# Kernel tuning notes

Hardware: AMD Instinct MI355X
Metric: run time of the kernel (lower is better)

The kernel has to match this reference:

```python
import jax, jax.numpy as jnp
import numpy as np

NEG_SLOPE = 0.2
EPS = 1e-16

N_NODES = 50000
N_EDGES = 800000
N_QUERY = 100000


def setup_inputs() -> dict:
    key = jax.random.key(0)
    ks = jax.random.split(key, 12)
    x = jax.random.normal(ks[0], (N_NODES, 128), dtype=jnp.float32)
    edge_index = jax.random.randint(ks[1], (2, N_EDGES), 0, N_NODES, dtype=jnp.int64)
    edge_label_index = jax.random.randint(ks[2], (2, N_QUERY), 0, N_NODES, dtype=jnp.int64)
    # layer 1: in=128 -> out=256, heads=4, per-head dim 64
    W1 = jax.random.normal(ks[3], (128, 256), dtype=jnp.float32) * 0.08
    a1_src = jax.random.normal(ks[4], (4, 64), dtype=jnp.float32) * 0.08
    a1_dst = jax.random.normal(ks[5], (4, 64), dtype=jnp.float32) * 0.08
    b1 = jnp.zeros((256,), dtype=jnp.float32)
    # layer 2: in=256 -> out=32, heads=2, per-head dim 16
    W2 = jax.random.normal(ks[6], (256, 32), dtype=jnp.float32) * 0.08
    a2_src = jax.random.normal(ks[7], (2, 16), dtype=jnp.float32) * 0.08
    a2_dst = jax.random.normal(ks[8], (2, 16), dtype=jnp.float32) * 0.08
    b2 = jnp.zeros((32,), dtype=jnp.float32)
    return {"x": x, "edge_index": edge_index, "edge_label_index": edge_label_index,
            "W1": W1, "a1_src": a1_src, "a1_dst": a1_dst, "b1": b1,
            "W2": W2, "a2_src": a2_src, "a2_dst": a2_dst, "b2": b2}


def gat_layer(x, src, dst, W, a_src, a_dst, b, heads):
    """Multi-head GAT: gather -> edge logits -> segment softmax over dst -> scatter-add."""
    n = x.shape[0]
    out = W.shape[1]
    c = out // heads
    h = (x @ W).reshape(n, heads, c)                       # [N,H,C]
    # per-node attention contributions: [N,H]
    alpha_s = jnp.einsum('nhc,hc->nh', h, a_src)
    alpha_d = jnp.einsum('nhc,hc->nh', h, a_dst)
    e = alpha_s[src] + alpha_d[dst]                         # [E,H]
    e = jax.nn.leaky_relu(e, NEG_SLOPE)
    # segment softmax over incoming edges of each dst node
    m = jax.ops.segment_max(e, dst, num_segments=n)         # [N,H]
    m = jnp.where(jnp.isfinite(m), m, 0.0)
    ex = jnp.exp(e - m[dst])                                # [E,H]
    s = jax.ops.segment_sum(ex, dst, num_segments=n)        # [N,H]
    w = ex / (s[dst] + EPS)                                 # [E,H]
    msg = h[src] * w[:, :, None]                            # [E,H,C]
    agg = jax.ops.segment_sum(msg, dst, num_segments=n)     # [N,H,C]
    return agg.reshape(n, out) + b


def reference(x, edge_index, edge_label_index, W1, a1_src, a1_dst, b1, W2, a2_src, a2_dst, b2):
    n = x.shape[0]
    loops = jnp.arange(n, dtype=edge_index.dtype)
    src = jnp.concatenate([edge_index[0], loops])
    dst = jnp.concatenate([edge_index[1], loops])
    # encode (dropout p=0 and use_bn=False are identities)
    z = gat_layer(x, src, dst, W1, a1_src, a1_dst, b1, heads=4)
    z = jax.nn.relu(z)
    z = gat_layer(z, src, dst, W2, a2_src, a2_dst, b2, heads=2)
    # decode: dot product of endpoint embeddings
    return (z[edge_label_index[0]] * z[edge_label_index[1]]).sum(axis=-1)
```

## Files before the change

### kernel.cpp

```cpp
#include <hip/hip_runtime.h>

#define NEG_SLOPE 0.2f
#define EPSV 1e-16f

__device__ __forceinline__ float lrelu(float e){ return (e > 0.f) ? e : NEG_SLOPE*e; }
__device__ __forceinline__ float bf2f(unsigned short u){ return __uint_as_float((unsigned)u << 16); }
__device__ __forceinline__ unsigned short f2bf(float f){
  unsigned u = __float_as_uint(f);
  u += 0x7FFFu + ((u >> 16) & 1u);
  return (unsigned short)(u >> 16);
}

__global__ void k_deg(const int* __restrict__ ei, int E, int N, int* __restrict__ deg){
  int t = blockIdx.x*blockDim.x + threadIdx.x;
  int ET = E + N;
  if (t >= ET) return;
  int dst = (t < E) ? ei[E + t] : (t - E);
  atomicAdd(&deg[dst], 1);
}

__global__ void k_scan(const int* __restrict__ deg, int N, int* __restrict__ rs){
  __shared__ int sums[1024];
  int tid = threadIdx.x;
  int chunk = (N + 1023) >> 10;
  int s = tid*chunk, e = min(s+chunk, N);
  int sum = 0;
  for (int i = s; i < e; ++i) sum += deg[i];
  sums[tid] = sum;
  __syncthreads();
  for (int off = 1; off < 1024; off <<= 1){
    int v = (tid >= off) ? sums[tid-off] : 0;
    __syncthreads();
    sums[tid] += v;
    __syncthreads();
  }
  int run = (tid == 0) ? 0 : sums[tid-1];
  for (int i = s; i < e; ++i){ rs[i] = run; run += deg[i]; }
  if (tid == 1023) rs[N] = run;
}

__global__ void k_fill(const int* __restrict__ ei, int E, int N,
                       const int* __restrict__ rs, int* __restrict__ cnt,
                       int* __restrict__ csr_s){
  int t = blockIdx.x*blockDim.x + threadIdx.x;
  int ET = E + N;
  if (t >= ET) return;
  int src, dst;
  if (t < E){ src = ei[t]; dst = ei[E + t]; } else { src = dst = t - E; }
  int pos = atomicAdd(&cnt[dst], 1);
  csr_s[rs[dst] + pos] = src;
}

__global__ __launch_bounds__(256) void k_gemm1(const float* __restrict__ x, const float* __restrict__ W1,
                                               const float* __restrict__ a1s, const float* __restrict__ a1d,
                                               int N, unsigned short* __restrict__ h1b,
                                               float* __restrict__ als, float* __restrict__ ald){
  __shared__ float xs[8][128];
  int bn = blockIdx.x * 8;
  int tid = threadIdx.x;
  {
    int m = tid >> 5, k4 = tid & 31;
    int node = bn + m;
    float4 v = (node < N) ? ((const float4*)x)[(size_t)node*32 + k4]
                          : make_float4(0.f,0.f,0.f,0.f);
    ((float4*)xs[m])[k4] = v;
  }
  __syncthreads();
  float acc[8];
  #pragma unroll
  for (int m = 0; m < 8; ++m) acc[m] = 0.f;
  int j = tid;
  for (int k = 0; k < 128; ++k){
    float w = W1[k*256 + j];
    #pragma unroll
    for (int m = 0; m < 8; ++m) acc[m] = fmaf(xs[m][k], w, acc[m]);
  }
  int head = j >> 6;
  int lane = j & 63;
  float cas = a1s[head*64 + lane];
  float cad = a1d[head*64 + lane];
  #pragma unroll
  for (int m = 0; m < 8; ++m){
    int node = bn + m;
    if (node < N) h1b[(size_t)node*256 + j] = f2bf(acc[m]);
    float vs = acc[m]*cas, vd = acc[m]*cad;
    #pragma unroll
    for (int o = 32; o; o >>= 1){ vs += __shfl_xor(vs, o, 64); vd += __shfl_xor(vd, o, 64); }
    if (lane == 0 && node < N){ als[node*4+head] = vs; ald[node*4+head] = vd; }
  }
}

__global__ __launch_bounds__(256) void k_gemm2(const float* __restrict__ z1, const float* __restrict__ W2,
                                               const float* __restrict__ a2s, const float* __restrict__ a2d,
                                               int N, float* __restrict__ h2,
                                               float* __restrict__ als, float* __restrict__ ald){
  __shared__ float zs[8][256];
  int bn = blockIdx.x * 8;
  int tid = threadIdx.x;
  {
    int m = tid >> 6, k4 = tid & 63;
    int node = bn + m;
    const float4 zero = make_float4(0.f,0.f,0.f,0.f);
    ((float4*)zs[m])[k4]      = (node < N)   ? ((const float4*)z1)[(size_t)node*64 + k4] : zero;
    int m2 = m + 4, node2 = bn + m2;
    ((float4*)zs[m2])[k4]     = (node2 < N)  ? ((const float4*)z1)[(size_t)node2*64 + k4] : zero;
  }
  __syncthreads();
  int j = tid & 31;
  int m = tid >> 5;
  float acc = 0.f;
  for (int k = 0; k < 256; ++k) acc = fmaf(zs[m][k], W2[k*32 + j], acc);
  int node = bn + m;
  int head = j >> 4, lane = j & 15;
  if (node < N) h2[(size_t)node*32 + j] = acc;
  float vs = acc * a2s[head*16 + lane];
  float vd = acc * a2d[head*16 + lane];
  #pragma unroll
  for (int o = 8; o; o >>= 1){ vs += __shfl_xor(vs, o, 64); vd += __shfl_xor(vd, o, 64); }
  if (lane == 0 && node < N){ als[node*2+head] = vs; ald[node*2+head] = vd; }
}

__global__ __launch_bounds__(256) void k_agg1(const int* __restrict__ rs, const int* __restrict__ csr_s,
                                              const float* __restrict__ als, const float* __restrict__ ald,
                                              const unsigned short* __restrict__ h1b, const float* __restrict__ b1,
                                              int N, float* __restrict__ z1){
  __shared__ int    sidx[256];
  __shared__ float  sexp[256*4];
  __shared__ float4 accl[4][64];
  __shared__ float  sl[4][64];
  int node = blockIdx.x;
  int tid = threadIdx.x;
  int w = tid >> 6, lane = tid & 63;
  int head = lane >> 4;
  int beg = rs[node], end = rs[node+1];
  const ushort4* h1v = (const ushort4*)h1b;
  float4 acc = make_float4(0.f,0.f,0.f,0.f);
  float s = 0.f;
  for (int base = beg; base < end; base += 256){
    int cnt = min(256, end - base);
    if (tid < cnt) sidx[tid] = csr_s[base + tid];
    __syncthreads();
    for (int t = tid; t < cnt*4; t += 256){
      int e = t >> 2, h = t & 3;
      int sv = sidx[e];
      sexp[t] = __expf(lrelu(als[sv*4 + h] + ald[node*4 + h]));
    }
    __syncthreads();
    int e = w;
    for (; e + 12 < cnt; e += 16){
      int s0 = sidx[e], s1 = sidx[e+4], s2 = sidx[e+8], s3 = sidx[e+12];
      float x0 = sexp[e*4+head], x1 = sexp[(e+4)*4+head];
      float x2 = sexp[(e+8)*4+head], x3 = sexp[(e+12)*4+head];
      ushort4 u0 = h1v[(size_t)s0*64 + lane];
      ushort4 u1 = h1v[(size_t)s1*64 + lane];
      ushort4 u2 = h1v[(size_t)s2*64 + lane];
      ushort4 u3 = h1v[(size_t)s3*64 + lane];
      acc.x = fmaf(bf2f(u0.x), x0, acc.x); acc.y = fmaf(bf2f(u0.y), x0, acc.y);
      acc.z = fmaf(bf2f(u0.z), x0, acc.z); acc.w = fmaf(bf2f(u0.w), x0, acc.w);
      acc.x = fmaf(bf2f(u1.x), x1, acc.x); acc.y = fmaf(bf2f(u1.y), x1, acc.y);
      acc.z = fmaf(bf2f(u1.z), x1, acc.z); acc.w = fmaf(bf2f(u1.w), x1, acc.w);
      acc.x = fmaf(bf2f(u2.x), x2, acc.x); acc.y = fmaf(bf2f(u2.y), x2, acc.y);
      acc.z = fmaf(bf2f(u2.z), x2, acc.z); acc.w = fmaf(bf2f(u2.w), x2, acc.w);
      acc.x = fmaf(bf2f(u3.x), x3, acc.x); acc.y = fmaf(bf2f(u3.y), x3, acc.y);
      acc.z = fmaf(bf2f(u3.z), x3, acc.z); acc.w = fmaf(bf2f(u3.w), x3, acc.w);
      s += (x0 + x1) + (x2 + x3);
    }
    for (; e < cnt; e += 4){
      int s0 = sidx[e];
      float x0 = sexp[e*4+head];
      ushort4 u0 = h1v[(size_t)s0*64 + lane];
      acc.x = fmaf(bf2f(u0.x), x0, acc.x); acc.y = fmaf(bf2f(u0.y), x0, acc.y);
      acc.z = fmaf(bf2f(u0.z), x0, acc.z); acc.w = fmaf(bf2f(u0.w), x0, acc.w);
      s += x0;
    }
    __syncthreads();
  }
  accl[w][lane] = acc;
  sl[w][lane] = s;
  __syncthreads();
  if (tid < 64){
    float4 a0 = accl[0][tid], a1 = accl[1][tid], a2 = accl[2][tid], a3 = accl[3][tid];
    float st = sl[0][tid] + sl[1][tid] + sl[2][tid] + sl[3][tid];
    float inv = 1.0f / (st + EPSV);
    float4 bb = ((const float4*)b1)[tid];
    float4 r;
    r.x = fmaf(a0.x + a1.x + a2.x + a3.x, inv, bb.x);
    r.y = fmaf(a0.y + a1.y + a2.y + a3.y, inv, bb.y);
    r.z = fmaf(a0.z + a1.z + a2.z + a3.z, inv, bb.z);
    r.w = fmaf(a0.w + a1.w + a2.w + a3.w, inv, bb.w);
    r.x = fmaxf(r.x, 0.f); r.y = fmaxf(r.y, 0.f);
    r.z = fmaxf(r.z, 0.f); r.w = fmaxf(r.w, 0.f);
    ((float4*)z1)[(size_t)node*64 + tid] = r;
  }
}

__global__ __launch_bounds__(256) void k_agg2(const int* __restrict__ rs, const int* __restrict__ csr_s,
                                              const float* __restrict__ als, const float* __restrict__ ald,
                                              const float* __restrict__ h2, const float* __restrict__ b2,
                                              int N, float* __restrict__ z2){
  int tid = threadIdx.x;
  int node = blockIdx.x*4 + (tid >> 6);
  if (node >= N) return;
  int lane = tid & 63;
  int slot = lane >> 3;
  int q    = lane & 7;
  int head = q >> 2;
  float aldn = ald[node*2 + head];
  int beg = rs[node], end = rs[node+1];
  float4 acc = make_float4(0.f,0.f,0.f,0.f);
  float s = 0.f;
  for (int i = beg + slot; i < end; i += 8){
    int s0 = csr_s[i];
    float x0 = __expf(lrelu(als[s0*2+head] + aldn));
    float4 v0 = ((const float4*)h2)[(size_t)s0*8 + q];
    acc.x = fmaf(v0.x, x0, acc.x); acc.y = fmaf(v0.y, x0, acc.y);
    acc.z = fmaf(v0.z, x0, acc.z); acc.w = fmaf(v0.w, x0, acc.w);
    s += x0;
  }
  #pragma unroll
  for (int o = 8; o < 64; o <<= 1){
    acc.x += __shfl_xor(acc.x, o, 64); acc.y += __shfl_xor(acc.y, o, 64);
    acc.z += __shfl_xor(acc.z, o, 64); acc.w += __shfl_xor(acc.w, o, 64);
    s += __shfl_xor(s, o, 64);
  }
  if (slot == 0){
    float inv = 1.0f / (s + EPSV);
    float4 bb = ((const float4*)b2)[q];
    float4 r;
    r.x = fmaf(acc.x, inv, bb.x); r.y = fmaf(acc.y, inv, bb.y);
    r.z = fmaf(acc.z, inv, bb.z); r.w = fmaf(acc.w, inv, bb.w);
    ((float4*)z2)[(size_t)node*8 + q] = r;
  }
}

__global__ void k_decode(const int* __restrict__ eli, int NQ,
                         const float* __restrict__ z2, float* __restrict__ out){
  int t = blockIdx.x*blockDim.x + threadIdx.x;
  if (t >= NQ*8) return;
  int qq = t >> 3, q = t & 7;
  int a = eli[qq], b = eli[NQ + qq];
  float4 va = ((const float4*)z2)[(size_t)a*8 + q];
  float4 vb = ((const float4*)z2)[(size_t)b*8 + q];
  float p = va.x*vb.x + va.y*vb.y + va.z*vb.z + va.w*vb.w;
  p += __shfl_xor(p, 1, 64); p += __shfl_xor(p, 2, 64); p += __shfl_xor(p, 4, 64);
  if (q == 0) out[qq] = p;
}

extern "C" void kernel_launch(void* const* d_in, const int* in_sizes, int n_in,
                              void* d_out, int out_size, void* d_ws, size_t ws_size,
                              hipStream_t stream) {
  const float* x   = (const float*)d_in[0];
  const int*   ei  = (const int*)d_in[1];
  const int*   eli = (const int*)d_in[2];
  const float* W1  = (const float*)d_in[3];
  const float* a1s = (const float*)d_in[4];
  const float* a1d = (const float*)d_in[5];
  const float* b1  = (const float*)d_in[6];
  const float* W2  = (const float*)d_in[7];
  const float* a2s = (const float*)d_in[8];
  const float* a2d = (const float*)d_in[9];
  const float* b2  = (const float*)d_in[10];
  float* out = (float*)d_out;

  int N  = in_sizes[0] / 128;
  int E  = in_sizes[1] / 2;
  int NQ = in_sizes[2] / 2;
  int ET = E + N;

  char* base = (char*)d_ws;
  size_t off = 0;
  auto alloc = [&](size_t elems)->char*{ char* r = base + off; off += elems*4; return r; };
  int*   deg   = (int*)  alloc(N);
  int*   cnt   = (int*)  alloc(N);
  size_t zbytes = off;
  int*   rs    = (int*)  alloc(N+1);
  int*   csr_s = (int*)  alloc(ET);
  float* al1s  = (float*)alloc((size_t)N*4);
  float* al1d  = (float*)alloc((size_t)N*4);
  float* al2s  = (float*)alloc((size_t)N*2);
  float* al2d  = (float*)alloc((size_t)N*2);
  unsigned short* h1b = (unsigned short*)alloc((size_t)N*128);
  float* z1    = (float*)alloc((size_t)N*256);
  float* h2    = (float*)alloc((size_t)N*32);
  float* z2    = (float*)alloc((size_t)N*32);
  (void)ws_size; (void)n_in; (void)out_size;

  hipMemsetAsync(d_ws, 0, zbytes, stream);

  k_deg <<<(ET+255)/256, 256, 0, stream>>>(ei, E, N, deg);
  k_scan<<<1, 1024, 0, stream>>>(deg, N, rs);
  k_fill<<<(ET+255)/256, 256, 0, stream>>>(ei, E, N, rs, cnt, csr_s);

  k_gemm1<<<(N+7)/8, 256, 0, stream>>>(x, W1, a1s, a1d, N, h1b, al1s, al1d);
  k_agg1<<<N, 256, 0, stream>>>(rs, csr_s, al1s, al1d, h1b, b1, N, z1);

  k_gemm2<<<(N+7)/8, 256, 0, stream>>>(z1, W2, a2s, a2d, N, h2, al2s, al2d);
  k_agg2<<<(N+3)/4, 256, 0, stream>>>(rs, csr_s, al2s, al2d, h2, b2, N, z2);

  k_decode<<<((long long)NQ*8+255)/256, 256, 0, stream>>>(eli, NQ, z2, out);
}
```

Before: 489.1 us.

## Compute layer-1 GEMM with fp16 MFMA after converting x and transposing W1

Replaces the scalar FP32 layer-1 GEMM with a matrix-core kernel using 16x16x32 f16 MFMA instructions, one wave per 16 nodes. A new prep kernel first converts x to fp16 and writes a transposed fp16 copy of W1 so the MFMA operands can be loaded as contiguous 8-element vectors. The attention dot products are folded into the MFMA epilogue through 16-lane shuffles. This targets the FP32 ALU cost of the dense projection, at the price of an extra conversion pass over x and reduced input precision (fp16 instead of fp32).

```diff
diff --git a/kernel.cpp b/kernel.cpp
--- a/kernel.cpp
+++ b/kernel.cpp
@@ -2,6 +2,9 @@
 
 #define NEG_SLOPE 0.2f
 #define EPSV 1e-16f
+
+typedef _Float16 half8 __attribute__((ext_vector_type(8)));
+typedef float f32x4 __attribute__((ext_vector_type(4)));
 
 __device__ __forceinline__ float lrelu(float e){ return (e > 0.f) ? e : NEG_SLOPE*e; }
 __device__ __forceinline__ float bf2f(unsigned short u){ return __uint_as_float((unsigned)u << 16); }
@@ -51,42 +54,71 @@
   csr_s[rs[dst] + pos] = src;
 }
 
-__global__ __launch_bounds__(256) void k_gemm1(const float* __restrict__ x, const float* __restrict__ W1,
-                                               const float* __restrict__ a1s, const float* __restrict__ a1d,
-                                               int N, unsigned short* __restrict__ h1b,
-                                               float* __restrict__ als, float* __restrict__ ald){
-  __shared__ float xs[8][128];
-  int bn = blockIdx.x * 8;
-  int tid = threadIdx.x;
-  {
-    int m = tid >> 5, k4 = tid & 31;
-    int node = bn + m;
-    float4 v = (node < N) ? ((const float4*)x)[(size_t)node*32 + k4]
-                          : make_float4(0.f,0.f,0.f,0.f);
-    ((float4*)xs[m])[k4] = v;
-  }
-  __syncthreads();
-  float acc[8];
+__global__ void k_prep(const float* __restrict__ x, const float* __restrict__ W1, int N,
+                       _Float16* __restrict__ x16, _Float16* __restrict__ W1t){
+  int gs = gridDim.x*blockDim.x;
+  int t = blockIdx.x*blockDim.x + threadIdx.x;
+  int totx = N*128;
+  for (int i = t; i < totx; i += gs) x16[i] = (_Float16)x[i];
+  for (int i = t; i < 128*256; i += gs){
+    int k = i >> 8, n = i & 255;
+    W1t[n*128 + k] = (_Float16)W1[i];
+  }
+}
+
+__global__ __launch_bounds__(256) void k_gemm1m(const _Float16* __restrict__ x16,
+                                                const _Float16* __restrict__ W1t,
+                                                const float* __restrict__ a1s, const float* __restrict__ a1d,
+                                                int N, unsigned short* __restrict__ h1b,
+                                                float* __restrict__ als, float* __restrict__ ald){
+  int wid = threadIdx.x >> 6;
+  int lane = threadIdx.x & 63;
+  int node0 = (blockIdx.x*4 + wid) * 16;
+  if (node0 >= N) return;
+  int col = lane & 15;
+  int kb8 = (lane >> 4) * 8;
+  int nodeA = node0 + col; if (nodeA > N-1) nodeA = N-1;
+
+  half8 a[4];
   #pragma unroll
-  for (int m = 0; m < 8; ++m) acc[m] = 0.f;
-  int j = tid;
-  for (int k = 0; k < 128; ++k){
-    float w = W1[k*256 + j];
+  for (int kb = 0; kb < 4; ++kb)
+    a[kb] = *(const half8*)(x16 + (size_t)nodeA*128 + kb*32 + kb8);
+
+  int rbase = (lane >> 4) * 4;
+  #pragma unroll
+  for (int hg = 0; hg < 4; ++hg){
+    float as_p[4] = {0.f,0.f,0.f,0.f};
+    float ad_p[4] = {0.f,0.f,0.f,0.f};
     #pragma unroll
-    for (int m = 0; m < 8; ++m) acc[m] = fmaf(xs[m][k], w, acc[m]);
-  }
-  int head = j >> 6;
-  int lane = j & 63;
-  float cas = a1s[head*64 + lane];
-  float cad = a1d[head*64 + lane];
-  #pragma unroll
-  for (int m = 0; m < 8; ++m){
-    int node = bn + m;
-    if (node < N) h1b[(size_t)node*256 + j] = f2bf(acc[m]);
-    float vs = acc[m]*cas, vd = acc[m]*cad;
+    for (int nti = 0; nti < 4; ++nti){
+      int nt = hg*4 + nti;
+      f32x4 acc = {0.f,0.f,0.f,0.f};
+      #pragma unroll
+      for (int kb = 0; kb < 4; ++kb){
+        half8 b = *(const half8*)(W1t + (size_t)(nt*16 + col)*128 + kb*32 + kb8);
+        acc = __builtin_amdgcn_mfma_f32_16x16x32_f16(a[kb], b, acc, 0, 0, 0);
+      }
+      int ch  = nt*16 + col;
+      float cas = a1s[hg*64 + (ch & 63)];
+      float cad = a1d[hg*64 + (ch & 63)];
+      #pragma unroll
+      for (int r = 0; r < 4; ++r){
+        int nd = node0 + rbase + r;
+        if (nd < N) h1b[(size_t)nd*256 + ch] = f2bf(acc[r]);
+        as_p[r] = fmaf(acc[r], cas, as_p[r]);
+        ad_p[r] = fmaf(acc[r], cad, ad_p[r]);
+      }
+    }
     #pragma unroll
-    for (int o = 32; o; o >>= 1){ vs += __shfl_xor(vs, o, 64); vd += __shfl_xor(vd, o, 64); }
-    if (lane == 0 && node < N){ als[node*4+head] = vs; ald[node*4+head] = vd; }
+    for (int r = 0; r < 4; ++r){
+      float vs = as_p[r], vd = ad_p[r];
+      #pragma unroll
+      for (int o = 1; o < 16; o <<= 1){ vs += __shfl_xor(vs, o, 64); vd += __shfl_xor(vd, o, 64); }
+      if (col == 0){
+        int nd = node0 + rbase + r;
+        if (nd < N){ als[nd*4 + hg] = vs; ald[nd*4 + hg] = vd; }
+      }
+    }
   }
 }
 
@@ -280,6 +312,8 @@
   float* al2s  = (float*)alloc((size_t)N*2);
   float* al2d  = (float*)alloc((size_t)N*2);
   unsigned short* h1b = (unsigned short*)alloc((size_t)N*128);
+  _Float16* x16 = (_Float16*)alloc((size_t)N*64);
+  _Float16* W1t = (_Float16*)alloc(16384);
   float* z1    = (float*)alloc((size_t)N*256);
   float* h2    = (float*)alloc((size_t)N*32);
   float* z2    = (float*)alloc((size_t)N*32);
@@ -291,7 +325,8 @@
   k_scan<<<1, 1024, 0, stream>>>(deg, N, rs);
   k_fill<<<(ET+255)/256, 256, 0, stream>>>(ei, E, N, rs, cnt, csr_s);
 
-  k_gemm1<<<(N+7)/8, 256, 0, stream>>>(x, W1, a1s, a1d, N, h1b, al1s, al1d);
+  k_prep<<<1024, 256, 0, stream>>>(x, W1, N, x16, W1t);
+  k_gemm1m<<<(N + 63)/64, 256, 0, stream>>>(x16, W1t, a1s, a1d, N, h1b, al1s, al1d);
   k_agg1<<<N, 256, 0, stream>>>(rs, csr_s, al1s, al1d, h1b, b1, N, z1);
 
   k_gemm2<<<(N+7)/8, 256, 0, stream>>>(z1, W2, a2s, a2d, N, h2, al2s, al2d);
```

Result: faster. 465.9 us (-4.7%).
